# Optimization experiments

Measured on AMD Instinct MI355X. Metric: run time of the kernel, lower is better.

Reference implementation:

```python
import jax, jax.numpy as jnp
import numpy as np

B, C, H, W = 2048, 256, 7, 7
EPS = 1e-6  # torch.nn.CosineSimilarity eps


def _masked_cos_loss(f1, f2, A):
    """Fused all-pairs masked cosine similarity.
    f1, f2: [B, C, H, W]; A: [H, W, H, W] binary mask.
    Replaces the original 7x7x7x7 Python loop of per-pixel CosineSimilarity calls.
    Returns per-batch loss [B]: sum_{ijkl: A==1} cos(f1[:,:,i,j], f2[:,:,k,l]) / (H*W*H*W).
    """
    n1 = jnp.linalg.norm(f1, axis=1)  # [B, H, W]
    n2 = jnp.linalg.norm(f2, axis=1)  # [B, H, W]
    dot = jnp.einsum('bcij,bckl->bijkl', f1, f2)  # [B, H, W, H, W]
    denom = jnp.maximum(n1[:, :, :, None, None] * n2[:, None, None, :, :], EPS)
    cos = dot / denom
    mask = (A == 1).astype(f1.dtype)
    return jnp.einsum('bijkl,ijkl->b', cos, mask) / (H * W * H * W)


def setup_inputs() -> dict:
    key = jax.random.key(0)
    k1, k2, k3, k4 = jax.random.split(key, 4)
    base_feature = jax.random.normal(k1, (B, C, H, W), dtype=jnp.float32)
    moment_feature = jax.random.normal(k2, (B, C, H, W), dtype=jnp.float32)
    base_A = jax.random.randint(k3, (H, W, H, W), 0, 2, dtype=jnp.int32)
    moment_A = jax.random.randint(k4, (H, W, H, W), 0, 2, dtype=jnp.int32)
    return {"base_feature": base_feature, "moment_feature": moment_feature,
            "base_A": base_A, "moment_A": moment_A}


def reference(base_feature, moment_feature, base_A, moment_A):
    # base_loss  = masked cos(base[i,j],   moment[k,l]) under base_A
    # moment_loss = masked cos(moment[i,j], base[k,l])  under moment_A
    base_loss = _masked_cos_loss(base_feature, moment_feature, base_A)
    moment_loss = _masked_cos_loss(moment_feature, base_feature, moment_A)
    return -base_loss - moment_loss  # [B]
```

## Files before the change

kernel.cpp:

```cpp
#include <hip/hip_runtime.h>
#include <math.h>


constexpr int NB     = 2048;
constexpr int NC     = 256;
constexpr int NP     = 49;
constexpr int SLAB_C = 16;
constexpr int SLAB_F = SLAB_C * NP;
constexpr int NSLAB  = NC / SLAB_C;
constexpr float EPS  = 1e-6f;

__global__ __launch_bounds__(256, 2)
void pixpro_kernel(const float* __restrict__ gbase,
                   const float* __restrict__ gmom,
                   const int*   __restrict__ A1,
                   const int*   __restrict__ A2,
                   float*       __restrict__ out)
{
    __shared__ float wt[NP * NP];
    __shared__ __align__(16) float slab[4][2 * SLAB_F];

    const int tid  = threadIdx.x;
    const int wave = tid >> 6;
    const int lane = tid & 63;
    const int b    = blockIdx.x * 4 + wave;

    for (int t = tid; t < NP * NP; t += 256) {
        int p = t / NP, q = t - p * NP;
        wt[t] = (A1[t] == 1 ? 1.0f : 0.0f) + (A2[q * NP + p] == 1 ? 1.0f : 0.0f);
    }
    __syncthreads();

    float* sl = slab[wave];

    const int lp = lane & 7, lq = lane >> 3;
    const int p0 = (lp < 7 ? lp : 6) * 7;
    const int q0 = (lq < 7 ? lq : 6) * 7;

    const float* gb = gbase + (size_t)b * (NC * NP);
    const float* gm = gmom  + (size_t)b * (NC * NP);

    const float* vA = sl + ((lane < NP) ? lane : (SLAB_F - NP + lane));
    const float* vB = sl + (SLAB_F + 15 + (lane < 34 ? lane : 33));
    const float* bp = sl + p0;
    const float* mp = sl + SLAB_F + q0;

    float acc[7][7];
    #pragma unroll
    for (int j = 0; j < 7; ++j)
        #pragma unroll
        for (int i = 0; i < 7; ++i) acc[j][i] = 0.0f;
    float nrm0 = 0.0f, nrm1 = 0.0f;

    float4 rb0 = {}, rb1 = {}, rb2 = {}, rb3 = {};
    float4 rm0 = {}, rm1 = {}, rm2 = {}, rm3 = {};
    {
        const float4* pb = (const float4*)gb;
        const float4* pm = (const float4*)gm;
        rb0 = pb[lane]; rb1 = pb[lane + 64]; rb2 = pb[lane + 128];
        rm0 = pm[lane]; rm1 = pm[lane + 64]; rm2 = pm[lane + 128];
        if (lane < 4) { rb3 = pb[lane + 192]; rm3 = pm[lane + 192]; }
    }

    for (int s = 0; s < NSLAB; ++s) {
        {
            float4* lb = (float4*)sl;
            float4* lm = (float4*)(sl + SLAB_F);
            lb[lane] = rb0; lb[lane + 64] = rb1; lb[lane + 128] = rb2;
            lm[lane] = rm0; lm[lane + 64] = rm1; lm[lane + 128] = rm2;
            if (lane < 4) { lb[lane + 192] = rb3; lm[lane + 192] = rm3; }
        }
        if (s + 1 < NSLAB) {
            const float4* pb = (const float4*)(gb + (s + 1) * SLAB_F);
            const float4* pm = (const float4*)(gm + (s + 1) * SLAB_F);
            rb0 = pb[lane]; rb1 = pb[lane + 64]; rb2 = pb[lane + 128];
            rm0 = pm[lane]; rm1 = pm[lane + 64]; rm2 = pm[lane + 128];
            if (lane < 4) { rb3 = pb[lane + 192]; rm3 = pm[lane + 192]; }
        }
        __syncthreads();

        #pragma unroll
        for (int c = 0; c < SLAB_C; ++c) {
            float bv[7], mv[7];
            #pragma unroll
            for (int i = 0; i < 7; ++i) bv[i] = bp[c * NP + i];
            #pragma unroll
            for (int j = 0; j < 7; ++j) mv[j] = mp[c * NP + j];
            float v0 = vA[c * NP];
            float v1 = vB[c * NP];
            nrm0 = fmaf(v0, v0, nrm0);
            nrm1 = fmaf(v1, v1, nrm1);
            #pragma unroll
            for (int j = 0; j < 7; ++j)
                #pragma unroll
                for (int i = 0; i < 7; ++i)
                    acc[j][i] = fmaf(bv[i], mv[j], acc[j][i]);
        }
        __syncthreads();
    }

    float* nsq = sl;
    nsq[lane] = nrm0;
    if (lane < 34) nsq[64 + lane] = nrm1;
    __syncthreads();

    float nbv[7], nmv[7];
    #pragma unroll
    for (int i = 0; i < 7; ++i) nbv[i] = sqrtf(nsq[p0 + i]);
    #pragma unroll
    for (int j = 0; j < 7; ++j) nmv[j] = sqrtf(nsq[NP + q0 + j]);

    float sum = 0.0f;
    if (lp < 7 && lq < 7) {
        #pragma unroll
        for (int j = 0; j < 7; ++j) {
            #pragma unroll
            for (int i = 0; i < 7; ++i) {
                float w     = wt[(p0 + i) * NP + (q0 + j)];
                float denom = fmaxf(nbv[i] * nmv[j], EPS);
                sum += w * acc[j][i] / denom;
            }
        }
    }

    #pragma unroll
    for (int m = 32; m; m >>= 1) sum += __shfl_xor(sum, m, 64);

    if (lane == 0) out[b] = sum * (-1.0f / 2401.0f);
}

extern "C" void kernel_launch(void* const* d_in, const int* in_sizes, int n_in,
                              void* d_out, int out_size, void* d_ws, size_t ws_size,
                              hipStream_t stream)
{
    (void)in_sizes; (void)n_in; (void)d_ws; (void)ws_size; (void)out_size;
    const float* base = (const float*)d_in[0];
    const float* mom  = (const float*)d_in[1];
    const int*   A1   = (const int*)d_in[2];
    const int*   A2   = (const int*)d_in[3];
    float*       out  = (float*)d_out;

    pixpro_kernel<<<NB / 4, 256, 0, stream>>>(base, mom, A1, A2, out);
}
```

Before: 243.1 us.

## Split channels across two waves per batch and pad LDS for vector reads

Each block now handles one batch element with two waves, and each wave accumulates the 49x49 dot products over half of the channels. The partial dot products and squared norms are combined through shared memory in the epilogue. The slab is stored in LDS with 8-float pixel rows, so each channel's 7-pixel row can be read with float4/float2 loads. The per-slab barriers are dropped because each wave only touches its own slab. The mask weights are now read straight from global memory instead of a precomputed shared table. The intent is more blocks and shorter per-wave chains, at the cost of a shared-memory reduction, redundant epilogue work in both waves, and dependence on wave-lockstep LDS ordering.

```diff
diff --git a/kernel.cpp b/kernel.cpp
--- a/kernel.cpp
+++ b/kernel.cpp
@@ -2,48 +2,67 @@
 #include <math.h>
 
 
-constexpr int NB     = 2048;
-constexpr int NC     = 256;
-constexpr int NP     = 49;
-constexpr int SLAB_C = 16;
-constexpr int SLAB_F = SLAB_C * NP;
-constexpr int NSLAB  = NC / SLAB_C;
-constexpr float EPS  = 1e-6f;
+constexpr int NB      = 2048;
+constexpr int NC      = 256;
+constexpr int NPIX    = 49;
+constexpr int SLOTS   = 56;
+constexpr int SLAB_C  = 16;
+constexpr int HALF    = SLAB_C * SLOTS;
+constexpr int SLABF   = SLAB_C * NPIX;
+constexpr int NS      = 8;
+constexpr int WCH     = NS * SLAB_C;
+constexpr float EPS   = 1e-6f;
 
-__global__ __launch_bounds__(256, 2)
+constexpr int SMEM_FLOATS = 2 * 2401 + 2 * 98;
+
+__device__ __forceinline__ int slot_of(int p) { return ((p / 7) << 3) + (p % 7); }
+
+__device__ __forceinline__ void scat4(float* st, int base, int r, float4 v) {
+    st[base]                = v.x;
+    st[base + 1 + (r >= 6)] = v.y;
+    st[base + 2 + (r >= 5)] = v.z;
+    st[base + 3 + (r >= 4)] = v.w;
+}
+
+__global__ __launch_bounds__(128, 4)
 void pixpro_kernel(const float* __restrict__ gbase,
                    const float* __restrict__ gmom,
                    const int*   __restrict__ A1,
                    const int*   __restrict__ A2,
                    float*       __restrict__ out)
 {
-    __shared__ float wt[NP * NP];
-    __shared__ __align__(16) float slab[4][2 * SLAB_F];
+    __shared__ __align__(16) float smem[SMEM_FLOATS];
 
     const int tid  = threadIdx.x;
     const int wave = tid >> 6;
     const int lane = tid & 63;
-    const int b    = blockIdx.x * 4 + wave;
+    const int b    = blockIdx.x;
 
-    for (int t = tid; t < NP * NP; t += 256) {
-        int p = t / NP, q = t - p * NP;
-        wt[t] = (A1[t] == 1 ? 1.0f : 0.0f) + (A2[q * NP + p] == 1 ? 1.0f : 0.0f);
-    }
-    __syncthreads();
-
-    float* sl = slab[wave];
+    float* st = smem + wave * (2 * HALF);
 
     const int lp = lane & 7, lq = lane >> 3;
-    const int p0 = (lp < 7 ? lp : 6) * 7;
-    const int q0 = (lq < 7 ? lq : 6) * 7;
+    const int lpc = (lp < 7 ? lp : 6), lqc = (lq < 7 ? lq : 6);
+    const int p0 = lpc * 7, q0 = lqc * 7;
 
-    const float* gb = gbase + (size_t)b * (NC * NP);
-    const float* gm = gmom  + (size_t)b * (NC * NP);
+    const float* gb = gbase + (size_t)b * (NC * NPIX) + wave * (WCH * NPIX);
+    const float* gm = gmom  + (size_t)b * (NC * NPIX) + wave * (WCH * NPIX);
 
-    const float* vA = sl + ((lane < NP) ? lane : (SLAB_F - NP + lane));
-    const float* vB = sl + (SLAB_F + 15 + (lane < 34 ? lane : 33));
-    const float* bp = sl + p0;
-    const float* mp = sl + SLAB_F + q0;
+    int wb[4], wr[4];
+    {
+        int f3 = 768 + ((lane < 4) ? lane * 4 : 12);
+        int fs[4] = { lane * 4, lane * 4 + 256, lane * 4 + 512, f3 };
+        #pragma unroll
+        for (int n = 0; n < 4; ++n) {
+            int f = fs[n], c = f / NPIX, p = f - c * NPIX;
+            wb[n] = c * SLOTS + slot_of(p);
+            wr[n] = p % 7;
+        }
+    }
+
+    const float* vA = st + ((lane < NPIX) ? slot_of(lane) : HALF + slot_of(lane - NPIX));
+    const float* vB = st + HALF + slot_of(lane < 34 ? 15 + lane : 48);
+    const float* bp = st + 8 * lpc;
+    const float* mp = st + HALF + 8 * lqc;
 
     float acc[7][7];
     #pragma unroll
@@ -52,8 +71,7 @@
         for (int i = 0; i < 7; ++i) acc[j][i] = 0.0f;
     float nrm0 = 0.0f, nrm1 = 0.0f;
 
-    float4 rb0 = {}, rb1 = {}, rb2 = {}, rb3 = {};
-    float4 rm0 = {}, rm1 = {}, rm2 = {}, rm3 = {};
+    float4 rb0, rb1, rb2, rb3 = {}, rm0, rm1, rm2, rm3 = {};
     {
         const float4* pb = (const float4*)gb;
         const float4* pm = (const float4*)gm;
@@ -62,32 +80,34 @@
         if (lane < 4) { rb3 = pb[lane + 192]; rm3 = pm[lane + 192]; }
     }
 
-    for (int s = 0; s < NSLAB; ++s) {
-        {
-            float4* lb = (float4*)sl;
-            float4* lm = (float4*)(sl + SLAB_F);
-            lb[lane] = rb0; lb[lane + 64] = rb1; lb[lane + 128] = rb2;
-            lm[lane] = rm0; lm[lane + 64] = rm1; lm[lane + 128] = rm2;
-            if (lane < 4) { lb[lane + 192] = rb3; lm[lane + 192] = rm3; }
-        }
-        if (s + 1 < NSLAB) {
-            const float4* pb = (const float4*)(gb + (s + 1) * SLAB_F);
-            const float4* pm = (const float4*)(gm + (s + 1) * SLAB_F);
+    for (int s = 0; s < NS; ++s) {
+        scat4(st, wb[0], wr[0], rb0);  scat4(st + HALF, wb[0], wr[0], rm0);
+        scat4(st, wb[1], wr[1], rb1);  scat4(st + HALF, wb[1], wr[1], rm1);
+        scat4(st, wb[2], wr[2], rb2);  scat4(st + HALF, wb[2], wr[2], rm2);
+        if (lane < 4) { scat4(st, wb[3], wr[3], rb3); scat4(st + HALF, wb[3], wr[3], rm3); }
+
+        if (s + 1 < NS) {
+            const float4* pb = (const float4*)(gb + (s + 1) * SLABF);
+            const float4* pm = (const float4*)(gm + (s + 1) * SLABF);
             rb0 = pb[lane]; rb1 = pb[lane + 64]; rb2 = pb[lane + 128];
             rm0 = pm[lane]; rm1 = pm[lane + 64]; rm2 = pm[lane + 128];
             if (lane < 4) { rb3 = pb[lane + 192]; rm3 = pm[lane + 192]; }
         }
-        __syncthreads();
 
         #pragma unroll
         for (int c = 0; c < SLAB_C; ++c) {
-            float bv[7], mv[7];
-            #pragma unroll
-            for (int i = 0; i < 7; ++i) bv[i] = bp[c * NP + i];
-            #pragma unroll
-            for (int j = 0; j < 7; ++j) mv[j] = mp[c * NP + j];
-            float v0 = vA[c * NP];
-            float v1 = vB[c * NP];
+            const float* bc = bp + c * SLOTS;
+            const float* mc = mp + c * SLOTS;
+            float4 b03 = *(const float4*)bc;
+            float2 b45 = *(const float2*)(bc + 4);
+            float  b6  = bc[6];
+            float4 m03 = *(const float4*)mc;
+            float2 m45 = *(const float2*)(mc + 4);
+            float  m6  = mc[6];
+            float bv[7] = { b03.x, b03.y, b03.z, b03.w, b45.x, b45.y, b6 };
+            float mv[7] = { m03.x, m03.y, m03.z, m03.w, m45.x, m45.y, m6 };
+            float v0 = vA[c * SLOTS];
+            float v1 = vB[c * SLOTS];
             nrm0 = fmaf(v0, v0, nrm0);
             nrm1 = fmaf(v1, v1, nrm1);
             #pragma unroll
@@ -96,19 +116,33 @@
                 for (int i = 0; i < 7; ++i)
                     acc[j][i] = fmaf(bv[i], mv[j], acc[j][i]);
         }
-        __syncthreads();
     }
 
-    float* nsq = sl;
-    nsq[lane] = nrm0;
-    if (lane < 34) nsq[64 + lane] = nrm1;
     __syncthreads();
+
+    float* nsqw = smem + 2 * 2401 + wave * 98;
+    nsqw[lane] = nrm0;
+    if (lane < 34) nsqw[64 + lane] = nrm1;
+
+    float* accw = smem + wave * 2401;
+    if (lp < 7 && lq < 7) {
+        #pragma unroll
+        for (int j = 0; j < 7; ++j)
+            #pragma unroll
+            for (int i = 0; i < 7; ++i)
+                accw[(p0 + i) * NPIX + (q0 + j)] = acc[j][i];
+    }
+    __syncthreads();
+
+    const float* acco = smem + (1 - wave) * 2401;
+    const float* nsq0 = smem + 2 * 2401;
+    const float* nsq1 = nsq0 + 98;
 
     float nbv[7], nmv[7];
     #pragma unroll
-    for (int i = 0; i < 7; ++i) nbv[i] = sqrtf(nsq[p0 + i]);
+    for (int i = 0; i < 7; ++i) nbv[i] = sqrtf(nsq0[p0 + i] + nsq1[p0 + i]);
     #pragma unroll
-    for (int j = 0; j < 7; ++j) nmv[j] = sqrtf(nsq[NP + q0 + j]);
+    for (int j = 0; j < 7; ++j) nmv[j] = sqrtf(nsq0[NPIX + q0 + j] + nsq1[NPIX + q0 + j]);
 
     float sum = 0.0f;
     if (lp < 7 && lq < 7) {
@@ -116,9 +150,11 @@
         for (int j = 0; j < 7; ++j) {
             #pragma unroll
             for (int i = 0; i < 7; ++i) {
-                float w     = wt[(p0 + i) * NP + (q0 + j)];
-                float denom = fmaxf(nbv[i] * nmv[j], EPS);
-                sum += w * acc[j][i] / denom;
+                int pi = p0 + i, qj = q0 + j;
+                float d = acc[j][i] + acco[pi * NPIX + qj];
+                float w = (A1[pi * NPIX + qj] == 1 ? 1.0f : 0.0f)
+                        + (A2[qj * NPIX + pi] == 1 ? 1.0f : 0.0f);
+                sum += w * d / fmaxf(nbv[i] * nmv[j], EPS);
             }
         }
     }
@@ -126,7 +162,7 @@
     #pragma unroll
     for (int m = 32; m; m >>= 1) sum += __shfl_xor(sum, m, 64);
 
-    if (lane == 0) out[b] = sum * (-1.0f / 2401.0f);
+    if (tid == 0) out[b] = sum * (-1.0f / 2401.0f);
 }
 
 extern "C" void kernel_launch(void* const* d_in, const int* in_sizes, int n_in,
@@ -140,5 +176,5 @@
     const int*   A2   = (const int*)d_in[3];
     float*       out  = (float*)d_out;
 
-    pixpro_kernel<<<NB / 4, 256, 0, stream>>>(base, mom, A1, A2, out);
+    pixpro_kernel<<<NB, 128, 0, stream>>>(base, mom, A1, A2, out);
 }
```

After: 692.6 us. 185% more time.

## Split each batch's channel reduction across four waves with direct global loads

Applied to the files above, without the earlier changes.

Each block now handles one batch element instead of four. Its four waves split the channel dimension (strided by 4) and load overlapping 8-wide pixel tiles straight from global memory into registers with float4 loads, dropping the LDS slab staging and the per-slab barriers. Partial dot products and squared norms are merged into shared memory with atomicAdd, then the masked cosine sum is reduced across the whole block. The aim is more parallelism per batch element and fewer synchronisations, at the cost of shared-memory atomics, redundant compute in overlapping tiles, and possibly unaligned float4 global loads.

```diff
diff --git a/kernel.cpp b/kernel.cpp
--- a/kernel.cpp
+++ b/kernel.cpp
@@ -2,131 +2,138 @@
 #include <math.h>
 
 
-constexpr int NB     = 2048;
+constexpr int NBATCH = 2048;
 constexpr int NC     = 256;
 constexpr int NP     = 49;
-constexpr int SLAB_C = 16;
-constexpr int SLAB_F = SLAB_C * NP;
-constexpr int NSLAB  = NC / SLAB_C;
+constexpr int FPB    = NC * NP;
 constexpr float EPS  = 1e-6f;
 
-__global__ __launch_bounds__(256, 2)
+__device__ __forceinline__ int tile_start(int g, int s) {
+    if (g < 6) return 8 * g + s;
+    return (s > 0) ? (s - 4) : 48;
+}
+
+__device__ __forceinline__ void own_range(int g, int s, int& lo, int& hi) {
+    if (g < 6) { lo = 0; int h = 49 - (8 * g + s); hi = (h > 8) ? 8 : h; }
+    else if (s > 0) { lo = 4 - s; hi = 4; }
+    else { lo = 0; hi = 1; }
+}
+
+__global__ __launch_bounds__(256)
 void pixpro_kernel(const float* __restrict__ gbase,
                    const float* __restrict__ gmom,
                    const int*   __restrict__ A1,
                    const int*   __restrict__ A2,
                    float*       __restrict__ out)
 {
-    __shared__ float wt[NP * NP];
-    __shared__ __align__(16) float slab[4][2 * SLAB_F];
+    __shared__ float dots[NP * NP];
+    __shared__ float bn[NP];
+    __shared__ float mn[NP];
+    __shared__ float red[4];
 
     const int tid  = threadIdx.x;
     const int wave = tid >> 6;
     const int lane = tid & 63;
-    const int b    = blockIdx.x * 4 + wave;
+    const int b    = blockIdx.x;
 
-    for (int t = tid; t < NP * NP; t += 256) {
-        int p = t / NP, q = t - p * NP;
-        wt[t] = (A1[t] == 1 ? 1.0f : 0.0f) + (A2[q * NP + p] == 1 ? 1.0f : 0.0f);
+    for (int t = tid; t < NP * NP; t += 256) dots[t] = 0.0f;
+    if (tid < NP) { bn[tid] = 0.0f; mn[tid] = 0.0f; }
+    __syncthreads();
+
+    const int r = wave;
+    const int s = (4 - r) & 3;
+    const int lp = lane & 7, lq = lane >> 3;
+
+    const float* fb = gbase + (size_t)b * FPB;
+    const float* fm = gmom  + (size_t)b * FPB;
+
+    const float* pA; const float* pB; int tA, tB;
+    if (lp <= 6 && lq <= 6)      { pA = fb; tA = tile_start(lp, s); pB = fm; tB = tile_start(lq, s); }
+    else if (lp == 7 && lq <= 6) { int t = tile_start(lq, s); pA = fb; pB = fb; tA = t; tB = t; }
+    else if (lq == 7 && lp <= 6) { int t = tile_start(lp, s); pA = fm; pB = fm; tA = t; tB = t; }
+    else                         { int t = tile_start(6, s);  pA = fm; pB = fm; tA = t; tB = t; }
+
+    const float* aptr = pA + r * NP + tA;
+    const float* bptr = pB + r * NP + tB;
+
+    float acc[8][8];
+    #pragma unroll
+    for (int i = 0; i < 8; ++i)
+        #pragma unroll
+        for (int j = 0; j < 8; ++j) acc[i][j] = 0.0f;
+
+    float4 a0 = *(const float4*)(aptr);
+    float4 a1 = *(const float4*)(aptr + 4);
+    float4 c0 = *(const float4*)(bptr);
+    float4 c1 = *(const float4*)(bptr + 4);
+
+    for (int k = 1; k < NC / 4; ++k) {
+        const float* ap = aptr + k * (4 * NP);
+        const float* bp = bptr + k * (4 * NP);
+        float4 na0 = *(const float4*)(ap);
+        float4 na1 = *(const float4*)(ap + 4);
+        float4 nc0 = *(const float4*)(bp);
+        float4 nc1 = *(const float4*)(bp + 4);
+
+        float bv[8] = { a0.x, a0.y, a0.z, a0.w, a1.x, a1.y, a1.z, a1.w };
+        float mv[8] = { c0.x, c0.y, c0.z, c0.w, c1.x, c1.y, c1.z, c1.w };
+        #pragma unroll
+        for (int i = 0; i < 8; ++i)
+            #pragma unroll
+            for (int j = 0; j < 8; ++j)
+                acc[i][j] = fmaf(bv[i], mv[j], acc[i][j]);
+
+        a0 = na0; a1 = na1; c0 = nc0; c1 = nc1;
+    }
+    {
+        float bv[8] = { a0.x, a0.y, a0.z, a0.w, a1.x, a1.y, a1.z, a1.w };
+        float mv[8] = { c0.x, c0.y, c0.z, c0.w, c1.x, c1.y, c1.z, c1.w };
+        #pragma unroll
+        for (int i = 0; i < 8; ++i)
+            #pragma unroll
+            for (int j = 0; j < 8; ++j)
+                acc[i][j] = fmaf(bv[i], mv[j], acc[i][j]);
+    }
+
+    if (lp <= 6 && lq <= 6) {
+        int plo, phi, qlo, qhi;
+        own_range(lp, s, plo, phi);
+        own_range(lq, s, qlo, qhi);
+        const int tp = tile_start(lp, s), tq = tile_start(lq, s);
+        #pragma unroll
+        for (int i = 0; i < 8; ++i)
+            #pragma unroll
+            for (int j = 0; j < 8; ++j)
+                if (i >= plo && i < phi && j >= qlo && j < qhi)
+                    atomicAdd(&dots[(tp + i) * NP + (tq + j)], acc[i][j]);
+    } else if (lp == 7 && lq <= 6) {
+        int lo, hi; own_range(lq, s, lo, hi);
+        const int t = tile_start(lq, s);
+        #pragma unroll
+        for (int i = 0; i < 8; ++i)
+            if (i >= lo && i < hi) atomicAdd(&bn[t + i], acc[i][i]);
+    } else if (lq == 7 && lp <= 6) {
+        int lo, hi; own_range(lp, s, lo, hi);
+        const int t = tile_start(lp, s);
+        #pragma unroll
+        for (int i = 0; i < 8; ++i)
+            if (i >= lo && i < hi) atomicAdd(&mn[t + i], acc[i][i]);
     }
     __syncthreads();
 
-    float* sl = slab[wave];
-
-    const int lp = lane & 7, lq = lane >> 3;
-    const int p0 = (lp < 7 ? lp : 6) * 7;
-    const int q0 = (lq < 7 ? lq : 6) * 7;
-
-    const float* gb = gbase + (size_t)b * (NC * NP);
-    const float* gm = gmom  + (size_t)b * (NC * NP);
-
-    const float* vA = sl + ((lane < NP) ? lane : (SLAB_F - NP + lane));
-    const float* vB = sl + (SLAB_F + 15 + (lane < 34 ? lane : 33));
-    const float* bp = sl + p0;
-    const float* mp = sl + SLAB_F + q0;
-
-    float acc[7][7];
-    #pragma unroll
-    for (int j = 0; j < 7; ++j)
-        #pragma unroll
-        for (int i = 0; i < 7; ++i) acc[j][i] = 0.0f;
-    float nrm0 = 0.0f, nrm1 = 0.0f;
-
-    float4 rb0 = {}, rb1 = {}, rb2 = {}, rb3 = {};
-    float4 rm0 = {}, rm1 = {}, rm2 = {}, rm3 = {};
-    {
-        const float4* pb = (const float4*)gb;
-        const float4* pm = (const float4*)gm;
-        rb0 = pb[lane]; rb1 = pb[lane + 64]; rb2 = pb[lane + 128];
-        rm0 = pm[lane]; rm1 = pm[lane + 64]; rm2 = pm[lane + 128];
-        if (lane < 4) { rb3 = pb[lane + 192]; rm3 = pm[lane + 192]; }
-    }
-
-    for (int s = 0; s < NSLAB; ++s) {
-        {
-            float4* lb = (float4*)sl;
-            float4* lm = (float4*)(sl + SLAB_F);
-            lb[lane] = rb0; lb[lane + 64] = rb1; lb[lane + 128] = rb2;
-            lm[lane] = rm0; lm[lane + 64] = rm1; lm[lane + 128] = rm2;
-            if (lane < 4) { lb[lane + 192] = rb3; lm[lane + 192] = rm3; }
-        }
-        if (s + 1 < NSLAB) {
-            const float4* pb = (const float4*)(gb + (s + 1) * SLAB_F);
-            const float4* pm = (const float4*)(gm + (s + 1) * SLAB_F);
-            rb0 = pb[lane]; rb1 = pb[lane + 64]; rb2 = pb[lane + 128];
-            rm0 = pm[lane]; rm1 = pm[lane + 64]; rm2 = pm[lane + 128];
-            if (lane < 4) { rb3 = pb[lane + 192]; rm3 = pm[lane + 192]; }
-        }
-        __syncthreads();
-
-        #pragma unroll
-        for (int c = 0; c < SLAB_C; ++c) {
-            float bv[7], mv[7];
-            #pragma unroll
-            for (int i = 0; i < 7; ++i) bv[i] = bp[c * NP + i];
-            #pragma unroll
-            for (int j = 0; j < 7; ++j) mv[j] = mp[c * NP + j];
-            float v0 = vA[c * NP];
-            float v1 = vB[c * NP];
-            nrm0 = fmaf(v0, v0, nrm0);
-            nrm1 = fmaf(v1, v1, nrm1);
-            #pragma unroll
-            for (int j = 0; j < 7; ++j)
-                #pragma unroll
-                for (int i = 0; i < 7; ++i)
-                    acc[j][i] = fmaf(bv[i], mv[j], acc[j][i]);
-        }
-        __syncthreads();
-    }
-
-    float* nsq = sl;
-    nsq[lane] = nrm0;
-    if (lane < 34) nsq[64 + lane] = nrm1;
-    __syncthreads();
-
-    float nbv[7], nmv[7];
-    #pragma unroll
-    for (int i = 0; i < 7; ++i) nbv[i] = sqrtf(nsq[p0 + i]);
-    #pragma unroll
-    for (int j = 0; j < 7; ++j) nmv[j] = sqrtf(nsq[NP + q0 + j]);
-
     float sum = 0.0f;
-    if (lp < 7 && lq < 7) {
-        #pragma unroll
-        for (int j = 0; j < 7; ++j) {
-            #pragma unroll
-            for (int i = 0; i < 7; ++i) {
-                float w     = wt[(p0 + i) * NP + (q0 + j)];
-                float denom = fmaxf(nbv[i] * nmv[j], EPS);
-                sum += w * acc[j][i] / denom;
-            }
-        }
+    for (int e = tid; e < NP * NP; e += 256) {
+        int p = e / NP, q = e - p * NP;
+        float w = (A1[e] == 1 ? 1.0f : 0.0f) + (A2[q * NP + p] == 1 ? 1.0f : 0.0f);
+        float den = fmaxf(sqrtf(bn[p]) * sqrtf(mn[q]), EPS);
+        sum += w * dots[e] / den;
     }
 
     #pragma unroll
     for (int m = 32; m; m >>= 1) sum += __shfl_xor(sum, m, 64);
-
-    if (lane == 0) out[b] = sum * (-1.0f / 2401.0f);
+    if (lane == 0) red[wave] = sum;
+    __syncthreads();
+    if (tid == 0) out[b] = (red[0] + red[1] + red[2] + red[3]) * (-1.0f / 2401.0f);
 }
 
 extern "C" void kernel_launch(void* const* d_in, const int* in_sizes, int n_in,
@@ -140,5 +147,5 @@
     const int*   A2   = (const int*)d_in[3];
     float*       out  = (float*)d_out;
 
-    pixpro_kernel<<<NB / 4, 256, 0, stream>>>(base, mom, A1, A2, out);
+    pixpro_kernel<<<NBATCH, 256, 0, stream>>>(base, mom, A1, A2, out);
 }
```

Measured after the change: 350.7 us. 44.3% more time.

## Compute pairwise dots and norms with split-fp16 MFMA instead of scalar FMA

Applied to the files above, without the earlier changes.

Replaces the per-lane 7x7 fp32 FMA outer-product accumulation with 16x16x16 fp16 MFMA tiles covering a padded 64x64 pixel-pair matrix. Each fp32 value is split into hi and lo fp16 parts, and three MFMAs per tile approximate fp32 accuracy. Squared norms are also computed with MFMAs and read off the diagonal. The per-slab block barriers are dropped because each wave only uses its own LDS region. This trades a lot of VALU work for matrix-core throughput, at the cost of padding waste and extra register pressure. Accuracy is slightly reduced because the hi*lo-only split omits the lo*lo term and can underflow small residuals.

```diff
diff --git a/kernel.cpp b/kernel.cpp
--- a/kernel.cpp
+++ b/kernel.cpp
@@ -2,15 +2,33 @@
 #include <math.h>
 
 
-constexpr int NB     = 2048;
+typedef _Float16 half4 __attribute__((ext_vector_type(4)));
+typedef float f32x4 __attribute__((ext_vector_type(4)));
+
+constexpr int NBATCH = 2048;
 constexpr int NC     = 256;
 constexpr int NP     = 49;
+constexpr int FPB    = NC * NP;
 constexpr int SLAB_C = 16;
-constexpr int SLAB_F = SLAB_C * NP;
+constexpr int SLABF  = SLAB_C * NP;
 constexpr int NSLAB  = NC / SLAB_C;
+constexpr int WBUF   = 2 * SLABF + 64;
 constexpr float EPS  = 1e-6f;
 
-__global__ __launch_bounds__(256, 2)
+__device__ __forceinline__ void split16(float x, _Float16& h, _Float16& l) {
+    h = (_Float16)x;
+    l = (_Float16)(x - (float)h);
+}
+
+__device__ __forceinline__ float vsel(f32x4 v, int r) {
+    float x = v[0];
+    x = (r == 1) ? v[1] : x;
+    x = (r == 2) ? v[2] : x;
+    x = (r == 3) ? v[3] : x;
+    return x;
+}
+
+__global__ __launch_bounds__(256)
 void pixpro_kernel(const float* __restrict__ gbase,
                    const float* __restrict__ gmom,
                    const int*   __restrict__ A1,
@@ -18,7 +36,9 @@
                    float*       __restrict__ out)
 {
     __shared__ float wt[NP * NP];
-    __shared__ __align__(16) float slab[4][2 * SLAB_F];
+    __shared__ __align__(16) float slab[4][WBUF];
+    __shared__ float bnorm[4][64];
+    __shared__ float mnorm[4][64];
 
     const int tid  = threadIdx.x;
     const int wave = tid >> 6;
@@ -31,101 +51,123 @@
     }
     __syncthreads();
 
-    float* sl = slab[wave];
+    float* sb = slab[wave];
+    const float* gb = gbase + (size_t)b * FPB;
+    const float* gm = gmom  + (size_t)b * FPB;
 
-    const int lp = lane & 7, lq = lane >> 3;
-    const int p0 = (lp < 7 ? lp : 6) * 7;
-    const int q0 = (lq < 7 ? lq : 6) * 7;
+    const int m    = lane & 15;
+    const int quad = lane >> 4;
+    const int fbase = 196 * quad + m;
 
-    const float* gb = gbase + (size_t)b * (NC * NP);
-    const float* gm = gmom  + (size_t)b * (NC * NP);
+    f32x4 accD[4][4], accB[4], accM[4];
+    #pragma unroll
+    for (int i = 0; i < 4; ++i) {
+        #pragma unroll
+        for (int j = 0; j < 4; ++j) accD[i][j] = (f32x4)0.0f;
+        accB[i] = (f32x4)0.0f;
+        accM[i] = (f32x4)0.0f;
+    }
 
-    const float* vA = sl + ((lane < NP) ? lane : (SLAB_F - NP + lane));
-    const float* vB = sl + (SLAB_F + 15 + (lane < 34 ? lane : 33));
-    const float* bp = sl + p0;
-    const float* mp = sl + SLAB_F + q0;
-
-    float acc[7][7];
-    #pragma unroll
-    for (int j = 0; j < 7; ++j)
-        #pragma unroll
-        for (int i = 0; i < 7; ++i) acc[j][i] = 0.0f;
-    float nrm0 = 0.0f, nrm1 = 0.0f;
-
-    float4 rb0 = {}, rb1 = {}, rb2 = {}, rb3 = {};
-    float4 rm0 = {}, rm1 = {}, rm2 = {}, rm3 = {};
+    float4 rb[4] = {}, rm[4] = {};
     {
         const float4* pb = (const float4*)gb;
         const float4* pm = (const float4*)gm;
-        rb0 = pb[lane]; rb1 = pb[lane + 64]; rb2 = pb[lane + 128];
-        rm0 = pm[lane]; rm1 = pm[lane + 64]; rm2 = pm[lane + 128];
-        if (lane < 4) { rb3 = pb[lane + 192]; rm3 = pm[lane + 192]; }
+        rb[0] = pb[lane]; rb[1] = pb[64 + lane]; rb[2] = pb[128 + lane];
+        rm[0] = pm[lane]; rm[1] = pm[64 + lane]; rm[2] = pm[128 + lane];
+        if (lane < 4) { rb[3] = pb[192 + lane]; rm[3] = pm[192 + lane]; }
     }
 
     for (int s = 0; s < NSLAB; ++s) {
         {
-            float4* lb = (float4*)sl;
-            float4* lm = (float4*)(sl + SLAB_F);
-            lb[lane] = rb0; lb[lane + 64] = rb1; lb[lane + 128] = rb2;
-            lm[lane] = rm0; lm[lane + 64] = rm1; lm[lane + 128] = rm2;
-            if (lane < 4) { lb[lane + 192] = rb3; lm[lane + 192] = rm3; }
+            float4* lb = (float4*)sb;
+            float4* lm = (float4*)(sb + SLABF);
+            lb[lane] = rb[0]; lb[64 + lane] = rb[1]; lb[128 + lane] = rb[2];
+            lm[lane] = rm[0]; lm[64 + lane] = rm[1]; lm[128 + lane] = rm[2];
+            if (lane < 4) { lb[192 + lane] = rb[3]; lm[192 + lane] = rm[3]; }
         }
         if (s + 1 < NSLAB) {
-            const float4* pb = (const float4*)(gb + (s + 1) * SLAB_F);
-            const float4* pm = (const float4*)(gm + (s + 1) * SLAB_F);
-            rb0 = pb[lane]; rb1 = pb[lane + 64]; rb2 = pb[lane + 128];
-            rm0 = pm[lane]; rm1 = pm[lane + 64]; rm2 = pm[lane + 128];
-            if (lane < 4) { rb3 = pb[lane + 192]; rm3 = pm[lane + 192]; }
+            const float4* pb = (const float4*)(gb + (s + 1) * SLABF);
+            const float4* pm = (const float4*)(gm + (s + 1) * SLABF);
+            rb[0] = pb[lane]; rb[1] = pb[64 + lane]; rb[2] = pb[128 + lane];
+            rm[0] = pm[lane]; rm[1] = pm[64 + lane]; rm[2] = pm[128 + lane];
+            if (lane < 4) { rb[3] = pb[192 + lane]; rm[3] = pm[192 + lane]; }
         }
-        __syncthreads();
+
+        half4 Ah[4], Al[4], Bh[4], Bl[4];
+        #pragma unroll
+        for (int t = 0; t < 4; ++t) {
+            const int o = fbase + 16 * t;
+            float a0 = sb[o], a1 = sb[o + 49], a2 = sb[o + 98], a3 = sb[o + 147];
+            float c0 = sb[SLABF + o], c1 = sb[SLABF + o + 49],
+                  c2 = sb[SLABF + o + 98], c3 = sb[SLABF + o + 147];
+            _Float16 h, l;
+            split16(a0, h, l); Ah[t][0] = h; Al[t][0] = l;
+            split16(a1, h, l); Ah[t][1] = h; Al[t][1] = l;
+            split16(a2, h, l); Ah[t][2] = h; Al[t][2] = l;
+            split16(a3, h, l); Ah[t][3] = h; Al[t][3] = l;
+            split16(c0, h, l); Bh[t][0] = h; Bl[t][0] = l;
+            split16(c1, h, l); Bh[t][1] = h; Bl[t][1] = l;
+            split16(c2, h, l); Bh[t][2] = h; Bl[t][2] = l;
+            split16(c3, h, l); Bh[t][3] = h; Bl[t][3] = l;
+        }
 
         #pragma unroll
-        for (int c = 0; c < SLAB_C; ++c) {
-            float bv[7], mv[7];
+        for (int mt = 0; mt < 4; ++mt) {
             #pragma unroll
-            for (int i = 0; i < 7; ++i) bv[i] = bp[c * NP + i];
-            #pragma unroll
-            for (int j = 0; j < 7; ++j) mv[j] = mp[c * NP + j];
-            float v0 = vA[c * NP];
-            float v1 = vB[c * NP];
-            nrm0 = fmaf(v0, v0, nrm0);
-            nrm1 = fmaf(v1, v1, nrm1);
-            #pragma unroll
-            for (int j = 0; j < 7; ++j)
-                #pragma unroll
-                for (int i = 0; i < 7; ++i)
-                    acc[j][i] = fmaf(bv[i], mv[j], acc[j][i]);
+            for (int nt = 0; nt < 4; ++nt) {
+                accD[mt][nt] = __builtin_amdgcn_mfma_f32_16x16x16f16(Ah[mt], Bh[nt], accD[mt][nt], 0, 0, 0);
+                accD[mt][nt] = __builtin_amdgcn_mfma_f32_16x16x16f16(Ah[mt], Bl[nt], accD[mt][nt], 0, 0, 0);
+                accD[mt][nt] = __builtin_amdgcn_mfma_f32_16x16x16f16(Al[mt], Bh[nt], accD[mt][nt], 0, 0, 0);
+            }
         }
-        __syncthreads();
+        #pragma unroll
+        for (int t = 0; t < 4; ++t) {
+            accB[t] = __builtin_amdgcn_mfma_f32_16x16x16f16(Ah[t], Ah[t], accB[t], 0, 0, 0);
+            accB[t] = __builtin_amdgcn_mfma_f32_16x16x16f16(Ah[t], Al[t], accB[t], 0, 0, 0);
+            accB[t] = __builtin_amdgcn_mfma_f32_16x16x16f16(Al[t], Ah[t], accB[t], 0, 0, 0);
+            accM[t] = __builtin_amdgcn_mfma_f32_16x16x16f16(Bh[t], Bh[t], accM[t], 0, 0, 0);
+            accM[t] = __builtin_amdgcn_mfma_f32_16x16x16f16(Bh[t], Bl[t], accM[t], 0, 0, 0);
+            accM[t] = __builtin_amdgcn_mfma_f32_16x16x16f16(Bl[t], Bh[t], accM[t], 0, 0, 0);
+        }
     }
 
-    float* nsq = sl;
-    nsq[lane] = nrm0;
-    if (lane < 34) nsq[64 + lane] = nrm1;
+    float* bn = bnorm[wave];
+    float* mn = mnorm[wave];
+    {
+        const int r0 = m - 4 * quad;
+        if (r0 >= 0 && r0 < 4) {
+            #pragma unroll
+            for (int t = 0; t < 4; ++t) {
+                bn[16 * t + m] = vsel(accB[t], r0);
+                mn[16 * t + m] = vsel(accM[t], r0);
+            }
+        }
+    }
     __syncthreads();
 
-    float nbv[7], nmv[7];
+    float sum = 0.0f;
     #pragma unroll
-    for (int i = 0; i < 7; ++i) nbv[i] = sqrtf(nsq[p0 + i]);
-    #pragma unroll
-    for (int j = 0; j < 7; ++j) nmv[j] = sqrtf(nsq[NP + q0 + j]);
-
-    float sum = 0.0f;
-    if (lp < 7 && lq < 7) {
-        #pragma unroll
-        for (int j = 0; j < 7; ++j) {
+    for (int nt = 0; nt < 4; ++nt) {
+        const int qq = 16 * nt + m;
+        if (qq < NP) {
+            const float nmv = sqrtf(mn[qq]);
             #pragma unroll
-            for (int i = 0; i < 7; ++i) {
-                float w     = wt[(p0 + i) * NP + (q0 + j)];
-                float denom = fmaxf(nbv[i] * nmv[j], EPS);
-                sum += w * acc[j][i] / denom;
+            for (int mt = 0; mt < 4; ++mt) {
+                #pragma unroll
+                for (int r = 0; r < 4; ++r) {
+                    const int p = 16 * mt + 4 * quad + r;
+                    if (p < NP) {
+                        const float nbv = sqrtf(bn[p]);
+                        const float d   = accD[mt][nt][r];
+                        sum += wt[p * NP + qq] * d / fmaxf(nbv * nmv, EPS);
+                    }
+                }
             }
         }
     }
 
     #pragma unroll
-    for (int m = 32; m; m >>= 1) sum += __shfl_xor(sum, m, 64);
-
+    for (int sh = 32; sh; sh >>= 1) sum += __shfl_xor(sum, sh, 64);
     if (lane == 0) out[b] = sum * (-1.0f / 2401.0f);
 }
 
@@ -140,5 +182,5 @@
     const int*   A2   = (const int*)d_in[3];
     float*       out  = (float*)d_out;
 
-    pixpro_kernel<<<NB / 4, 256, 0, stream>>>(base, mom, A1, A2, out);
+    pixpro_kernel<<<NBATCH / 4, 256, 0, stream>>>(base, mom, A1, A2, out);
 }
```

After: 274.9 us. +13.1%, slower.
